# Kernel optimization log

Measured on AMD Instinct MI355X. Metric: run time of the kernel, lower is better.

The kernel has to match this reference:

```python
import jax, jax.numpy as jnp
import numpy as np

B, N, D = 4, 4096, 1024
H, DH = 16, 64  # heads, dim_head; inner_dim = H*DH = 1024
EPS = 1e-6


def setup_inputs() -> dict:
    key = jax.random.key(0)
    ks = jax.random.split(key, 6)
    s = 1.0 / np.sqrt(D)
    return {
        "x": jax.random.normal(ks[0], (B, N, D), dtype=jnp.float32),
        "Wq": jax.random.normal(ks[1], (D, H * DH), dtype=jnp.float32) * s,
        "Wk": jax.random.normal(ks[2], (D, H * DH), dtype=jnp.float32) * s,
        "Wv": jax.random.normal(ks[3], (D, H * DH), dtype=jnp.float32) * s,
        "Wo": jax.random.normal(ks[4], (H * DH, D), dtype=jnp.float32) * s,
        "bo": jnp.zeros((D,), dtype=jnp.float32),
    }


def reference(x, Wq, Wk, Wv, Wo, bo):
    # projections, split heads: b n (h d) -> b h n d
    def split_heads(t):
        b, n, _ = t.shape
        return t.reshape(b, n, H, DH).transpose(0, 2, 1, 3)

    q = split_heads(x @ Wq)
    k = split_heads(x @ Wk)  # context = x (self-attention)
    v = split_heads(x @ Wv)

    # elu feature map: elu(x) + 1
    q = jax.nn.elu(q) + 1.0
    k = jax.nn.elu(k) + 1.0

    # normalizer z[b,h,n,1] = q . sum_n k  + eps
    k_sum = k.sum(axis=2)                                  # b h d
    z = jnp.einsum('bhnd,bhd->bhn', q, k_sum)[..., None] + EPS

    # kv outer-product reduction: O(N d^2)
    kv = jnp.einsum('bhnd,bhne->bhde', k, v)               # b h d e
    out = jnp.einsum('bhnd,bhde->bhne', q, kv) / z         # b h n e

    # merge heads: b h n d -> b n (h d)
    out = out.transpose(0, 2, 1, 3).reshape(x.shape[0], x.shape[1], H * DH)
    return out @ Wo + bo
```

## Files before the change

kernel.cpp:

```cpp
#include <hip/hip_runtime.h>
#include <hip/hip_bf16.h>


#define DEV_INLINE __device__ __forceinline__

typedef short bf16x8 __attribute__((ext_vector_type(8)));
typedef float f32x4  __attribute__((ext_vector_type(4)));

static constexpr int Bb = 4, Nn = 4096, Dd = 1024, Hh = 16, DHd = 64;
static constexpr int Mrows = Bb * Nn;

DEV_INLINE float bf2f(short s) {
  unsigned u = ((unsigned)(unsigned short)s) << 16;
  float f; __builtin_memcpy(&f, &u, 4); return f;
}
DEV_INLINE short f2bf(float f) {
  unsigned u; __builtin_memcpy(&u, &f, 4);
  unsigned r = (u + 0x7fffu + ((u >> 16) & 1u)) >> 16;
  return (short)r;
}

DEV_INLINE void gload16(const void* g, void* l) {
  typedef __attribute__((address_space(1))) const void gv_t;
  typedef __attribute__((address_space(3))) void lv_t;
  __builtin_amdgcn_global_load_lds((gv_t*)g, (lv_t*)l, 16, 0, 0);
}

#define SBAR() __builtin_amdgcn_s_barrier()
#define WAITV(n) asm volatile("s_waitcnt vmcnt(" #n ")" ::: "memory")


__global__ void convert_x_kernel(const float* __restrict__ x, short* __restrict__ xb) {
  const int total = Mrows * 1024 / 4;
  for (int i = blockIdx.x * 256 + threadIdx.x; i < total; i += 2048 * 256) {
    float4 v = ((const float4*)x)[i];
    short4 o;
    o.x = f2bf(v.x); o.y = f2bf(v.y); o.z = f2bf(v.z); o.w = f2bf(v.w);
    ((short4*)xb)[i] = o;
  }
}

__global__ void transposeW_kernel(const float* __restrict__ Wq, const float* __restrict__ Wk,
                                  const float* __restrict__ Wv, const float* __restrict__ Wo,
                                  short* __restrict__ Wt, short* __restrict__ WoT) {
  int z = blockIdx.z;
  const float* W = (z == 0) ? Wq : (z == 1) ? Wk : (z == 2) ? Wv : Wo;
  short* dstb = (z < 3) ? (Wt + (size_t)z * 1024 * 1024) : WoT;
  __shared__ float tile[64][69];
  int t = threadIdx.x;
  int r = t >> 2, c4 = (t & 3) << 4;
  const float* src = W + (blockIdx.y * 64 + r) * 1024 + blockIdx.x * 64 + c4;
  for (int j = 0; j < 4; ++j) {
    float4 v = ((const float4*)src)[j];
    tile[r][c4 + 4 * j + 0] = v.x;
    tile[r][c4 + 4 * j + 1] = v.y;
    tile[r][c4 + 4 * j + 2] = v.z;
    tile[r][c4 + 4 * j + 3] = v.w;
  }
  __syncthreads();
  __attribute__((aligned(16))) short tmp[16];
  for (int j = 0; j < 16; ++j) tmp[j] = f2bf(tile[c4 + j][r]);
  short* dst = dstb + (blockIdx.x * 64 + r) * 1024 + blockIdx.y * 64 + c4;
  ((int4*)dst)[0] = ((int4*)tmp)[0];
  ((int4*)dst)[1] = ((int4*)tmp)[1];
}


DEV_INLINE void stage_half(const short* __restrict__ gtile, char* smreg, int h) {
  int t = threadIdx.x;
  int lane = t & 63, w = t >> 6;
#pragma unroll
  for (int l = 0; l < 2; ++l) {
    int rbase = h * 128 + l * 64 + w * 8;
    int row = rbase + (lane >> 3);
    int slot = lane & 7;
    gload16(gtile + (size_t)row * 1024 + ((slot ^ (row & 7)) << 3),
            smreg + (size_t)rbase * 128);
  }
}

#define READ_A(set, mbase, kk)                                                     \
  _Pragma("unroll") for (int m_ = 0; m_ < 4; ++m_) {                               \
    int row_ = wr * 128 + ((mbase) + m_) * 16 + rl;                                \
    int slot_ = (kk) * 4 + kg;                                                     \
    a[m_] = *(const bf16x8*)(smraw + (set) * 65536 + row_ * 128 +                  \
                             (((slot_ ^ (row_ & 7))) << 4));                       \
  }

#define READ_B(set, kk)                                                            \
  _Pragma("unroll") for (int n_ = 0; n_ < 4; ++n_) {                               \
    int row_ = wc * 64 + n_ * 16 + rl;                                             \
    int slot_ = (kk) * 4 + kg;                                                     \
    b[n_] = *(const bf16x8*)(smraw + 32768 + (set) * 65536 + row_ * 128 +          \
                             (((slot_ ^ (row_ & 7))) << 4));                       \
  }

#define MF(mbase)                                                                  \
  __builtin_amdgcn_s_setprio(1);                                                   \
  _Pragma("unroll") for (int m_ = 0; m_ < 4; ++m_)                                 \
    _Pragma("unroll") for (int n_ = 0; n_ < 4; ++n_)                               \
      acc[(mbase) + m_][n_] = __builtin_amdgcn_mfma_f32_16x16x32_bf16(             \
          a[m_], b[n_], acc[(mbase) + m_][n_], 0, 0, 0);                           \
  __builtin_amdgcn_s_setprio(0);

template <int MODE>
__global__ __launch_bounds__(512, 2) void gemm256_kernel(
    const short* __restrict__ A, const short* __restrict__ Bt,
    short* __restrict__ q, short* __restrict__ kT, short* __restrict__ vT,
    float* __restrict__ out, const float* __restrict__ bias, int nTilesN) {
  __shared__ __align__(16) char smraw[131072];
  char* smA0 = smraw;
  char* smB0 = smraw + 32768;
  char* smA1 = smraw + 65536;
  char* smB1 = smraw + 98304;

  int bid = blockIdx.x;
  int xcd = bid & 7, lo = bid >> 3;
  int tn = lo >> 3, tmg = lo & 7;
  int tm = xcd * 8 + tmg;

  int t = threadIdx.x, w = t >> 6, lane = t & 63;
  int rl = lane & 15, kg = lane >> 4;
  int wr = w >> 2, wc = w & 3;

  const short* Ab = A + (size_t)tm * 256 * 1024;
  const short* Bb2 = Bt + (size_t)tn * 256 * 1024;

  f32x4 acc[8][4] = {};
  bf16x8 a[4], b[4];

  stage_half(Ab, smA0, 0);
  stage_half(Ab, smA0, 1);
  stage_half(Bb2, smB0, 0);
  stage_half(Bb2, smB0, 1);
  stage_half(Bb2 + 64, smB1, 0);
  WAITV(2);
  SBAR();

#pragma unroll 1
  for (int i = 0; i < 8; ++i) {
    int k_odd = i * 128 + 64, k_n2 = i * 128 + 128, k_n3 = i * 128 + 192;
    READ_A(0, 0, 0); READ_B(0, 0);
    stage_half(Bb2 + k_odd, smB1, 1);
    SBAR(); MF(0); SBAR();
    READ_A(0, 4, 0);
    stage_half(Ab + k_odd, smA1, 0);
    SBAR(); MF(4); SBAR();
    READ_A(0, 0, 1); READ_B(0, 1);
    stage_half(Ab + k_odd, smA1, 1);
    SBAR(); MF(0); SBAR();
    READ_A(0, 4, 1);
    stage_half(Bb2 + k_n2, smB0, 0);
    WAITV(2); SBAR(); MF(4); SBAR();
    READ_A(1, 0, 0); READ_B(1, 0);
    stage_half(Ab + k_n2, smA0, 0);
    SBAR(); MF(0); SBAR();
    READ_A(1, 4, 0);
    stage_half(Ab + k_n2, smA0, 1);
    SBAR(); MF(4); SBAR();
    READ_A(1, 0, 1); READ_B(1, 1);
    stage_half(Bb2 + k_n2, smB0, 1);
    SBAR(); MF(0); SBAR();
    READ_A(1, 4, 1);
    stage_half(Bb2 + k_n3, smB1, 0);
    WAITV(2); SBAR(); MF(4); SBAR();
  }

  WAITV(0);
  SBAR();

  if (MODE == 1) {
    float* smf = (float*)smraw;
    for (int hp = 0; hp < 2; ++hp) {
      if (wr == hp) {
#pragma unroll
        for (int m = 0; m < 8; ++m)
#pragma unroll
          for (int n = 0; n < 4; ++n)
#pragma unroll
            for (int r = 0; r < 4; ++r) {
              int lrow = m * 16 + kg * 4 + r;
              int col = wc * 64 + n * 16 + rl;
              smf[lrow * 256 + ((((col >> 2) ^ (lrow & 7))) << 2) + (col & 3)] = acc[m][n][r];
            }
      }
      SBAR();
      for (int it = 0; it < 16; ++it) {
        int idx = it * 512 + t;
        int row = idx >> 6, c4 = (idx & 63) << 2;
        float4 v = *(const float4*)&smf[row * 256 + ((((c4 >> 2) ^ (row & 7))) << 2)];
        float4 bv = *(const float4*)&bias[tn * 256 + c4];
        v.x += bv.x; v.y += bv.y; v.z += bv.z; v.w += bv.w;
        *(float4*)&out[(size_t)(tm * 256 + hp * 128 + row) * Dd + tn * 256 + c4] = v;
      }
      SBAR();
    }
    return;
  }

  short* smc = (short*)smraw;
  int sec = tn >> 2, tl = tn & 3;
#pragma unroll
  for (int m = 0; m < 8; ++m)
#pragma unroll
    for (int n = 0; n < 4; ++n)
#pragma unroll
      for (int r = 0; r < 4; ++r) {
        float v = acc[m][n][r];
        if (sec <= 1) v = v > 0.f ? v + 1.f : __expf(v);
        int row = wr * 128 + m * 16 + kg * 4 + r;
        int col = wc * 64 + n * 16 + rl;
        int rr = (sec == 0) ? row : col;
        int cc = (sec == 0) ? col : row;
        smc[rr * 256 + ((((cc >> 3) ^ (rr & 7))) << 3) + (cc & 7)] = f2bf(v);
      }
  SBAR();
  if (sec == 0) {
    for (int it = 0; it < 16; ++it) {
      int idx = it * 512 + t;
      int row = idx >> 5, c8 = (idx & 31) << 3;
      int4 val = *(const int4*)&smc[row * 256 + ((((c8 >> 3) ^ (row & 7))) << 3)];
      int grow = tm * 256 + row;
      int bI = grow >> 12, n = grow & 4095;
      int g = tl * 256 + c8;
      int h = g >> 6, d0 = g & 63;
      *(int4*)&q[(((size_t)(bI * Hh + h)) * Nn + n) * DHd + d0] = val;
    }
  } else {
    short* dst = (sec == 1) ? kT : vT;
    for (int it = 0; it < 16; ++it) {
      int idx = it * 512 + t;
      int dr = idx >> 5, c8 = (idx & 31) << 3;
      int4 val = *(const int4*)&smc[dr * 256 + ((((c8 >> 3) ^ (dr & 7))) << 3)];
      int g = tl * 256 + dr;
      int h = g >> 6, d = g & 63;
      int grow0 = tm * 256 + c8;
      int bI = grow0 >> 12, n0 = grow0 & 4095;
      *(int4*)&dst[(((size_t)(bI * Hh + h)) * DHd + d) * Nn + n0] = val;
    }
  }
}

__global__ void ksum_kernel(const short* __restrict__ kT, float* __restrict__ ksp) {
  int bh = blockIdx.x >> 3, seg = blockIdx.x & 7;
  int t = threadIdx.x;
  int d = t >> 2, sub = t & 3;
  const short* row = kT + ((size_t)bh * DHd + d) * Nn + seg * 512;
  float s = 0.f;
  for (int i = sub * 8; i < 512; i += 32) {
    bf16x8 v = *(const bf16x8*)&row[i];
    for (int j = 0; j < 8; ++j) s += bf2f(v[j]);
  }
  s += __shfl_xor(s, 1);
  s += __shfl_xor(s, 2);
  if (sub == 0) ksp[(bh * 8 + seg) * 64 + d] = s;
}

__global__ __launch_bounds__(256, 2) void kv_kernel(const short* __restrict__ kT,
                                                    const short* __restrict__ vT,
                                                    float* __restrict__ kvp) {
  __shared__ __align__(16) short smK[64 * 128];
  __shared__ __align__(16) short smV[64 * 128];
  int bh = blockIdx.x, seg = blockIdx.y;
  int t = threadIdx.x;
  int w = t >> 6, lane = t & 63, rl = lane & 15, kg = lane >> 4;
  const short* kb = kT + (size_t)bh * DHd * Nn + seg * 1024;
  const short* vb = vT + (size_t)bh * DHd * Nn + seg * 1024;
  f32x4 acc[4] = {};
  for (int n0 = 0; n0 < 1024; n0 += 128) {
    __syncthreads();
    for (int p = 0; p < 4; ++p) {
      int c = p * 256 + t;
      int row = c >> 4, u = c & 15;
      int off = ((u ^ (row & 15)) << 3);
      gload16(kb + row * Nn + n0 + off, (char*)smK + p * 4096 + w * 1024);
      gload16(vb + row * Nn + n0 + off, (char*)smV + p * 4096 + w * 1024);
    }
    __syncthreads();
    for (int kk = 0; kk < 4; ++kk) {
      int slot = kk * 4 + kg;
      int rowA = w * 16 + rl;
      bf16x8 a = *(const bf16x8*)&smK[rowA * 128 + ((slot ^ (rowA & 15)) << 3)];
      for (int nt = 0; nt < 4; ++nt) {
        int rowB = nt * 16 + rl;
        bf16x8 b = *(const bf16x8*)&smV[rowB * 128 + ((slot ^ (rowB & 15)) << 3)];
        acc[nt] = __builtin_amdgcn_mfma_f32_16x16x32_bf16(a, b, acc[nt], 0, 0, 0);
      }
    }
  }
  float* smf = (float*)smK;
  __syncthreads();
  for (int nt = 0; nt < 4; ++nt)
    for (int r = 0; r < 4; ++r)
      smf[(nt * 16 + rl) * 64 + (w * 16 + kg * 4 + r)] = acc[nt][r];
  __syncthreads();
  float* dst = kvp + ((size_t)(bh * 4 + seg)) * 4096;
  for (int i = 0; i < 4; ++i) {
    int idx = i * 256 + t;
    int e = idx >> 4, c4 = (idx & 15) << 2;
    *(float4*)&dst[e * 64 + c4] = *(const float4*)&smf[e * 64 + c4];
  }
}

__global__ void kvc_kernel(const float* __restrict__ kvp, short* __restrict__ kvT) {
  int bh = blockIdx.x, t = threadIdx.x;
  const float* p0 = kvp + (size_t)bh * 4 * 4096;
  for (int rep = 0; rep < 4; ++rep) {
    int idx = rep * 1024 + t * 4;
    float4 a = *(const float4*)&p0[idx];
    float4 b = *(const float4*)&p0[4096 + idx];
    float4 c = *(const float4*)&p0[8192 + idx];
    float4 d = *(const float4*)&p0[12288 + idx];
    short4 o;
    o.x = f2bf(a.x + b.x + c.x + d.x);
    o.y = f2bf(a.y + b.y + c.y + d.y);
    o.z = f2bf(a.z + b.z + c.z + d.z);
    o.w = f2bf(a.w + b.w + c.w + d.w);
    *(short4*)&kvT[(size_t)bh * 4096 + idx] = o;
  }
}

__global__ __launch_bounds__(256, 2) void attn_kernel(const short* __restrict__ q,
                                                      const short* __restrict__ kvT,
                                                      const float* __restrict__ ksp,
                                                      short* __restrict__ attn) {
  int rb = blockIdx.x, bh = blockIdx.y;
  int b = bh >> 4, h = bh & 15;
  __shared__ float sks[64];
  __shared__ __align__(16) short satt[64 * 64];
  int t = threadIdx.x, w = t >> 6, lane = t & 63, rl = lane & 15, kg = lane >> 4;
  if (t < 64) {
    float s = 0.f;
    for (int j = 0; j < 8; ++j) s += ksp[(bh * 8 + j) * 64 + t];
    sks[t] = s;
  }
  __syncthreads();
  int row0 = rb * 64 + w * 16;
  const short* qb = q + ((size_t)bh * Nn + row0) * DHd;
  const short* kvb = kvT + (size_t)bh * 4096;
  f32x4 acc[4] = {};
  float zp = 0.f;
  for (int kk = 0; kk < 2; ++kk) {
    int kb = kk * 32 + kg * 8;
    bf16x8 a = *(const bf16x8*)&qb[rl * DHd + kb];
    for (int j = 0; j < 8; ++j) zp += bf2f(a[j]) * sks[kb + j];
    for (int nt = 0; nt < 4; ++nt) {
      bf16x8 bfr = *(const bf16x8*)&kvb[(nt * 16 + rl) * 64 + kb];
      acc[nt] = __builtin_amdgcn_mfma_f32_16x16x32_bf16(a, bfr, acc[nt], 0, 0, 0);
    }
  }
  zp += __shfl_xor(zp, 16);
  zp += __shfl_xor(zp, 32);
  float zr[4];
  for (int r = 0; r < 4; ++r) zr[r] = __shfl(zp, kg * 4 + r);
  for (int nt = 0; nt < 4; ++nt)
    for (int r = 0; r < 4; ++r)
      satt[(w * 16 + kg * 4 + r) * 64 + nt * 16 + rl] = f2bf(acc[nt][r] / (zr[r] + 1e-6f));
  __syncthreads();
  for (int i = 0; i < 2; ++i) {
    int idx = i * 256 + t;
    int row = idx >> 3, c8 = (idx & 7) << 3;
    int n = rb * 64 + row;
    *(int4*)&attn[((size_t)(b * Nn + n)) * 1024 + h * 64 + c8] = *(const int4*)&satt[row * 64 + c8];
  }
}

extern "C" void kernel_launch(void* const* d_in, const int* in_sizes, int n_in,
                              void* d_out, int out_size, void* d_ws, size_t ws_size,
                              hipStream_t stream) {
  const float* x  = (const float*)d_in[0];
  const float* Wq = (const float*)d_in[1];
  const float* Wk = (const float*)d_in[2];
  const float* Wv = (const float*)d_in[3];
  const float* Wo = (const float*)d_in[4];
  const float* bo = (const float*)d_in[5];
  float* out = (float*)d_out;

  char* ws = (char*)d_ws;
  size_t off = 0;
  auto alloc = [&](size_t bytes) {
    char* p = ws + off;
    off += (bytes + 255) & ~(size_t)255;
    return p;
  };
  short* xb   = (short*)alloc((size_t)Mrows * 1024 * 2);
  short* Wt   = (short*)alloc((size_t)3072 * 1024 * 2);
  short* WoT  = (short*)alloc((size_t)1024 * 1024 * 2);
  short* qb   = (short*)alloc((size_t)64 * Nn * DHd * 2);
  short* kT   = (short*)alloc((size_t)64 * DHd * Nn * 2);
  short* vT   = (short*)alloc((size_t)64 * DHd * Nn * 2);
  float* ksp  = (float*)alloc((size_t)64 * 8 * 64 * 4);
  float* kvp  = (float*)alloc((size_t)64 * 4 * 4096 * 4);
  short* kvT  = (short*)alloc((size_t)64 * 4096 * 2);
  short* attn = (short*)alloc((size_t)Mrows * 1024 * 2);
  (void)alloc(8192);

  convert_x_kernel<<<2048, 256, 0, stream>>>(x, xb);
  transposeW_kernel<<<dim3(16, 16, 4), 256, 0, stream>>>(Wq, Wk, Wv, Wo, Wt, WoT);

  gemm256_kernel<0><<<768, 512, 0, stream>>>(xb, Wt, qb, kT, vT, nullptr, nullptr, 12);
  ksum_kernel<<<512, 256, 0, stream>>>(kT, ksp);
  kv_kernel<<<dim3(64, 4), 256, 0, stream>>>(kT, vT, kvp);
  kvc_kernel<<<64, 256, 0, stream>>>(kvp, kvT);
  attn_kernel<<<dim3(64, 64), 256, 0, stream>>>(qb, kvT, ksp, attn);
  gemm256_kernel<1><<<256, 512, 0, stream>>>(attn, WoT, nullptr, nullptr, nullptr, out, bo, 4);
}
```

Baseline: 250.7 us.

## Fuse k-sum into QKV GEMM epilogue, precompute LDS addresses, split kv over more blocks

The k column sum moves into the QKV GEMM epilogue, which accumulates it with atomics into a buffer zeroed by the weight-transpose kernel. This removes the separate ksum kernel and its re-read of kT. The GEMM main loop now uses precomputed swizzled LDS base pointers and global offsets, cutting address arithmetic per tile step. The kv reduction is split into 8 segments instead of 4 for more parallelism, at the cost of a larger partial buffer to combine. Float atomics make the k sum order nondeterministic.

Measured after the change: 250.1 us. No clear change (-0.3%).

```diff
diff --git a/kernel.cpp b/kernel.cpp
--- a/kernel.cpp
+++ b/kernel.cpp
@@ -42,12 +42,15 @@
 
 __global__ void transposeW_kernel(const float* __restrict__ Wq, const float* __restrict__ Wk,
                                   const float* __restrict__ Wv, const float* __restrict__ Wo,
-                                  short* __restrict__ Wt, short* __restrict__ WoT) {
+                                  short* __restrict__ Wt, short* __restrict__ WoT,
+                                  float* __restrict__ ksum) {
   int z = blockIdx.z;
+  int t = threadIdx.x;
+  if (z == 0 && blockIdx.y == 0 && blockIdx.x < 16)
+    ksum[blockIdx.x * 256 + t] = 0.f;
   const float* W = (z == 0) ? Wq : (z == 1) ? Wk : (z == 2) ? Wv : Wo;
   short* dstb = (z < 3) ? (Wt + (size_t)z * 1024 * 1024) : WoT;
   __shared__ float tile[64][69];
-  int t = threadIdx.x;
   int r = t >> 2, c4 = (t & 3) << 4;
   const float* src = W + (blockIdx.y * 64 + r) * 1024 + blockIdx.x * 64 + c4;
   for (int j = 0; j < 4; ++j) {
@@ -66,53 +69,33 @@
 }
 
 
-DEV_INLINE void stage_half(const short* __restrict__ gtile, char* smreg, int h) {
-  int t = threadIdx.x;
-  int lane = t & 63, w = t >> 6;
-#pragma unroll
-  for (int l = 0; l < 2; ++l) {
-    int rbase = h * 128 + l * 64 + w * 8;
-    int row = rbase + (lane >> 3);
-    int slot = lane & 7;
-    gload16(gtile + (size_t)row * 1024 + ((slot ^ (row & 7)) << 3),
-            smreg + (size_t)rbase * 128);
-  }
-}
-
-#define READ_A(set, mbase, kk)                                                     \
-  _Pragma("unroll") for (int m_ = 0; m_ < 4; ++m_) {                               \
-    int row_ = wr * 128 + ((mbase) + m_) * 16 + rl;                                \
-    int slot_ = (kk) * 4 + kg;                                                     \
-    a[m_] = *(const bf16x8*)(smraw + (set) * 65536 + row_ * 128 +                  \
-                             (((slot_ ^ (row_ & 7))) << 4));                       \
-  }
-
-#define READ_B(set, kk)                                                            \
-  _Pragma("unroll") for (int n_ = 0; n_ < 4; ++n_) {                               \
-    int row_ = wc * 64 + n_ * 16 + rl;                                             \
-    int slot_ = (kk) * 4 + kg;                                                     \
-    b[n_] = *(const bf16x8*)(smraw + 32768 + (set) * 65536 + row_ * 128 +          \
-                             (((slot_ ^ (row_ & 7))) << 4));                       \
-  }
-
-#define MF(mbase)                                                                  \
-  __builtin_amdgcn_s_setprio(1);                                                   \
-  _Pragma("unroll") for (int m_ = 0; m_ < 4; ++m_)                                 \
-    _Pragma("unroll") for (int n_ = 0; n_ < 4; ++n_)                               \
-      acc[(mbase) + m_][n_] = __builtin_amdgcn_mfma_f32_16x16x32_bf16(             \
-          a[m_], b[n_], acc[(mbase) + m_][n_], 0, 0, 0);                           \
+#define RA(set, mbase, kk)                                                   \
+  _Pragma("unroll") for (int m_ = 0; m_ < 4; ++m_)                           \
+    a[m_] = *(const bf16x8*)(baseA##set##kk + ((mbase) + m_) * 2048);
+
+#define RB(set, kk)                                                          \
+  _Pragma("unroll") for (int n_ = 0; n_ < 4; ++n_)                           \
+    b[n_] = *(const bf16x8*)(baseB##set##kk + n_ * 2048);
+
+#define MF(mbase)                                                            \
+  __builtin_amdgcn_s_setprio(1);                                             \
+  _Pragma("unroll") for (int m_ = 0; m_ < 4; ++m_)                           \
+    _Pragma("unroll") for (int n_ = 0; n_ < 4; ++n_)                         \
+      acc[(mbase) + m_][n_] = __builtin_amdgcn_mfma_f32_16x16x32_bf16(       \
+          a[m_], b[n_], acc[(mbase) + m_][n_], 0, 0, 0);                     \
   __builtin_amdgcn_s_setprio(0);
+
+#define STG(Gb, t, h, reg)                                                   \
+  gload16((Gb) + (t) * 64 + (h) * 131072 + goff,         (reg) + (h) * 16384 + wq);          \
+  gload16((Gb) + (t) * 64 + (h) * 131072 + 65536 + goff, (reg) + (h) * 16384 + 8192 + wq);
 
 template <int MODE>
 __global__ __launch_bounds__(512, 2) void gemm256_kernel(
     const short* __restrict__ A, const short* __restrict__ Bt,
     short* __restrict__ q, short* __restrict__ kT, short* __restrict__ vT,
-    float* __restrict__ out, const float* __restrict__ bias, int nTilesN) {
+    float* __restrict__ out, const float* __restrict__ bias,
+    float* __restrict__ ksum, int nTilesN) {
   __shared__ __align__(16) char smraw[131072];
-  char* smA0 = smraw;
-  char* smB0 = smraw + 32768;
-  char* smA1 = smraw + 65536;
-  char* smB1 = smraw + 98304;
 
   int bid = blockIdx.x;
   int xcd = bid & 7, lo = bid >> 3;
@@ -126,43 +109,59 @@
   const short* Ab = A + (size_t)tm * 256 * 1024;
   const short* Bb2 = Bt + (size_t)tn * 256 * 1024;
 
+  const int rx = rl & 7;
+  char* baseA00 = smraw + (wr * 128 + rl) * 128 + (((0 * 4 + kg) ^ rx) << 4);
+  char* baseA01 = smraw + (wr * 128 + rl) * 128 + (((1 * 4 + kg) ^ rx) << 4);
+  char* baseA10 = baseA00 + 65536;
+  char* baseA11 = baseA01 + 65536;
+  char* baseB00 = smraw + 32768 + (wc * 64 + rl) * 128 + (((0 * 4 + kg) ^ rx) << 4);
+  char* baseB01 = smraw + 32768 + (wc * 64 + rl) * 128 + (((1 * 4 + kg) ^ rx) << 4);
+  char* baseB10 = baseB00 + 65536;
+  char* baseB11 = baseB01 + 65536;
+
+  int srow = w * 8 + (lane >> 3);
+  const int goff = srow * 1024 + (((lane & 7) ^ (srow & 7)) << 3);
+  const int wq = w * 1024;
+  char* regA0 = smraw;
+  char* regB0 = smraw + 32768;
+  char* regA1 = smraw + 65536;
+  char* regB1 = smraw + 98304;
+
   f32x4 acc[8][4] = {};
   bf16x8 a[4], b[4];
 
-  stage_half(Ab, smA0, 0);
-  stage_half(Ab, smA0, 1);
-  stage_half(Bb2, smB0, 0);
-  stage_half(Bb2, smB0, 1);
-  stage_half(Bb2 + 64, smB1, 0);
+  STG(Ab, 0, 0, regA0); STG(Ab, 0, 1, regA0);
+  STG(Bb2, 0, 0, regB0); STG(Bb2, 0, 1, regB0);
+  STG(Bb2, 1, 0, regB1);
   WAITV(2);
   SBAR();
 
 #pragma unroll 1
   for (int i = 0; i < 8; ++i) {
-    int k_odd = i * 128 + 64, k_n2 = i * 128 + 128, k_n3 = i * 128 + 192;
-    READ_A(0, 0, 0); READ_B(0, 0);
-    stage_half(Bb2 + k_odd, smB1, 1);
+    int t1 = 2 * i + 1, t2 = 2 * i + 2, t3 = 2 * i + 3;
+    RA(0, 0, 0); RB(0, 0);
+    STG(Bb2, t1, 1, regB1);
     SBAR(); MF(0); SBAR();
-    READ_A(0, 4, 0);
-    stage_half(Ab + k_odd, smA1, 0);
+    RA(0, 4, 0);
+    STG(Ab, t1, 0, regA1);
     SBAR(); MF(4); SBAR();
-    READ_A(0, 0, 1); READ_B(0, 1);
-    stage_half(Ab + k_odd, smA1, 1);
+    RA(0, 0, 1); RB(0, 1);
+    STG(Ab, t1, 1, regA1);
     SBAR(); MF(0); SBAR();
-    READ_A(0, 4, 1);
-    stage_half(Bb2 + k_n2, smB0, 0);
+    RA(0, 4, 1);
+    STG(Bb2, t2, 0, regB0);
     WAITV(2); SBAR(); MF(4); SBAR();
-    READ_A(1, 0, 0); READ_B(1, 0);
-    stage_half(Ab + k_n2, smA0, 0);
+    RA(1, 0, 0); RB(1, 0);
+    STG(Ab, t2, 0, regA0);
     SBAR(); MF(0); SBAR();
-    READ_A(1, 4, 0);
-    stage_half(Ab + k_n2, smA0, 1);
+    RA(1, 4, 0);
+    STG(Ab, t2, 1, regA0);
     SBAR(); MF(4); SBAR();
-    READ_A(1, 0, 1); READ_B(1, 1);
-    stage_half(Bb2 + k_n2, smB0, 1);
+    RA(1, 0, 1); RB(1, 1);
+    STG(Bb2, t2, 1, regB0);
     SBAR(); MF(0); SBAR();
-    READ_A(1, 4, 1);
-    stage_half(Bb2 + k_n3, smB1, 0);
+    RA(1, 4, 1);
+    STG(Bb2, t3, 0, regB1);
     WAITV(2); SBAR(); MF(4); SBAR();
   }
 
@@ -238,22 +237,20 @@
       int bI = grow0 >> 12, n0 = grow0 & 4095;
       *(int4*)&dst[(((size_t)(bI * Hh + h)) * DHd + d) * Nn + n0] = val;
     }
-  }
-}
-
-__global__ void ksum_kernel(const short* __restrict__ kT, float* __restrict__ ksp) {
-  int bh = blockIdx.x >> 3, seg = blockIdx.x & 7;
-  int t = threadIdx.x;
-  int d = t >> 2, sub = t & 3;
-  const short* row = kT + ((size_t)bh * DHd + d) * Nn + seg * 512;
-  float s = 0.f;
-  for (int i = sub * 8; i < 512; i += 32) {
-    bf16x8 v = *(const bf16x8*)&row[i];
-    for (int j = 0; j < 8; ++j) s += bf2f(v[j]);
-  }
-  s += __shfl_xor(s, 1);
-  s += __shfl_xor(s, 2);
-  if (sub == 0) ksp[(bh * 8 + seg) * 64 + d] = s;
+    if (sec == 1) {
+      int dcol = t >> 1, half = t & 1;
+      float s = 0.f;
+      for (int c = half * 128; c < half * 128 + 128; ++c)
+        s += bf2f(smc[dcol * 256 + ((((c >> 3) ^ (dcol & 7))) << 3) + (c & 7)]);
+      s += __shfl_xor(s, 1);
+      if (half == 0) {
+        int g = tl * 256 + dcol;
+        int h = g >> 6, d = g & 63;
+        int bI = (tm * 256) >> 12;
+        atomicAdd(&ksum[(bI * Hh + h) * DHd + d], s);
+      }
+    }
+  }
 }
 
 __global__ __launch_bounds__(256, 2) void kv_kernel(const short* __restrict__ kT,
@@ -264,10 +261,10 @@
   int bh = blockIdx.x, seg = blockIdx.y;
   int t = threadIdx.x;
   int w = t >> 6, lane = t & 63, rl = lane & 15, kg = lane >> 4;
-  const short* kb = kT + (size_t)bh * DHd * Nn + seg * 1024;
-  const short* vb = vT + (size_t)bh * DHd * Nn + seg * 1024;
+  const short* kb = kT + (size_t)bh * DHd * Nn + seg * 512;
+  const short* vb = vT + (size_t)bh * DHd * Nn + seg * 512;
   f32x4 acc[4] = {};
-  for (int n0 = 0; n0 < 1024; n0 += 128) {
+  for (int n0 = 0; n0 < 512; n0 += 128) {
     __syncthreads();
     for (int p = 0; p < 4; ++p) {
       int c = p * 256 + t;
@@ -280,11 +277,11 @@
     for (int kk = 0; kk < 4; ++kk) {
       int slot = kk * 4 + kg;
       int rowA = w * 16 + rl;
-      bf16x8 a = *(const bf16x8*)&smK[rowA * 128 + ((slot ^ (rowA & 15)) << 3)];
+      bf16x8 av = *(const bf16x8*)&smK[rowA * 128 + ((slot ^ (rowA & 15)) << 3)];
       for (int nt = 0; nt < 4; ++nt) {
         int rowB = nt * 16 + rl;
-        bf16x8 b = *(const bf16x8*)&smV[rowB * 128 + ((slot ^ (rowB & 15)) << 3)];
-        acc[nt] = __builtin_amdgcn_mfma_f32_16x16x32_bf16(a, b, acc[nt], 0, 0, 0);
+        bf16x8 bv = *(const bf16x8*)&smV[rowB * 128 + ((slot ^ (rowB & 15)) << 3)];
+        acc[nt] = __builtin_amdgcn_mfma_f32_16x16x32_bf16(av, bv, acc[nt], 0, 0, 0);
       }
     }
   }
@@ -294,7 +291,7 @@
     for (int r = 0; r < 4; ++r)
       smf[(nt * 16 + rl) * 64 + (w * 16 + kg * 4 + r)] = acc[nt][r];
   __syncthreads();
-  float* dst = kvp + ((size_t)(bh * 4 + seg)) * 4096;
+  float* dst = kvp + ((size_t)(bh * 8 + seg)) * 4096;
   for (int i = 0; i < 4; ++i) {
     int idx = i * 256 + t;
     int e = idx >> 4, c4 = (idx & 15) << 2;
@@ -304,36 +301,30 @@
 
 __global__ void kvc_kernel(const float* __restrict__ kvp, short* __restrict__ kvT) {
   int bh = blockIdx.x, t = threadIdx.x;
-  const float* p0 = kvp + (size_t)bh * 4 * 4096;
+  const float* p0 = kvp + (size_t)bh * 8 * 4096;
   for (int rep = 0; rep < 4; ++rep) {
     int idx = rep * 1024 + t * 4;
-    float4 a = *(const float4*)&p0[idx];
-    float4 b = *(const float4*)&p0[4096 + idx];
-    float4 c = *(const float4*)&p0[8192 + idx];
-    float4 d = *(const float4*)&p0[12288 + idx];
+    float4 s = *(const float4*)&p0[idx];
+    for (int j = 1; j < 8; ++j) {
+      float4 aa = *(const float4*)&p0[j * 4096 + idx];
+      s.x += aa.x; s.y += aa.y; s.z += aa.z; s.w += aa.w;
+    }
     short4 o;
-    o.x = f2bf(a.x + b.x + c.x + d.x);
-    o.y = f2bf(a.y + b.y + c.y + d.y);
-    o.z = f2bf(a.z + b.z + c.z + d.z);
-    o.w = f2bf(a.w + b.w + c.w + d.w);
+    o.x = f2bf(s.x); o.y = f2bf(s.y); o.z = f2bf(s.z); o.w = f2bf(s.w);
     *(short4*)&kvT[(size_t)bh * 4096 + idx] = o;
   }
 }
 
 __global__ __launch_bounds__(256, 2) void attn_kernel(const short* __restrict__ q,
                                                       const short* __restrict__ kvT,
-                                                      const float* __restrict__ ksp,
+                                                      const float* __restrict__ ksum,
                                                       short* __restrict__ attn) {
   int rb = blockIdx.x, bh = blockIdx.y;
   int b = bh >> 4, h = bh & 15;
   __shared__ float sks[64];
   __shared__ __align__(16) short satt[64 * 64];
   int t = threadIdx.x, w = t >> 6, lane = t & 63, rl = lane & 15, kg = lane >> 4;
-  if (t < 64) {
-    float s = 0.f;
-    for (int j = 0; j < 8; ++j) s += ksp[(bh * 8 + j) * 64 + t];
-    sks[t] = s;
-  }
+  if (t < 64) sks[t] = ksum[bh * 64 + t];
   __syncthreads();
   int row0 = rb * 64 + w * 16;
   const short* qb = q + ((size_t)bh * Nn + row0) * DHd;
@@ -342,11 +333,11 @@
   float zp = 0.f;
   for (int kk = 0; kk < 2; ++kk) {
     int kb = kk * 32 + kg * 8;
-    bf16x8 a = *(const bf16x8*)&qb[rl * DHd + kb];
-    for (int j = 0; j < 8; ++j) zp += bf2f(a[j]) * sks[kb + j];
+    bf16x8 av = *(const bf16x8*)&qb[rl * DHd + kb];
+    for (int j = 0; j < 8; ++j) zp += bf2f(av[j]) * sks[kb + j];
     for (int nt = 0; nt < 4; ++nt) {
       bf16x8 bfr = *(const bf16x8*)&kvb[(nt * 16 + rl) * 64 + kb];
-      acc[nt] = __builtin_amdgcn_mfma_f32_16x16x32_bf16(a, bfr, acc[nt], 0, 0, 0);
+      acc[nt] = __builtin_amdgcn_mfma_f32_16x16x32_bf16(av, bfr, acc[nt], 0, 0, 0);
     }
   }
   zp += __shfl_xor(zp, 16);
@@ -389,19 +380,18 @@
   short* qb   = (short*)alloc((size_t)64 * Nn * DHd * 2);
   short* kT   = (short*)alloc((size_t)64 * DHd * Nn * 2);
   short* vT   = (short*)alloc((size_t)64 * DHd * Nn * 2);
-  float* ksp  = (float*)alloc((size_t)64 * 8 * 64 * 4);
-  float* kvp  = (float*)alloc((size_t)64 * 4 * 4096 * 4);
+  float* ksum = (float*)alloc((size_t)64 * 64 * 4);
+  float* kvp  = (float*)alloc((size_t)64 * 8 * 4096 * 4);
   short* kvT  = (short*)alloc((size_t)64 * 4096 * 2);
   short* attn = (short*)alloc((size_t)Mrows * 1024 * 2);
-  (void)alloc(8192);
+  (void)alloc(1 << 20);
 
   convert_x_kernel<<<2048, 256, 0, stream>>>(x, xb);
-  transposeW_kernel<<<dim3(16, 16, 4), 256, 0, stream>>>(Wq, Wk, Wv, Wo, Wt, WoT);
-
-  gemm256_kernel<0><<<768, 512, 0, stream>>>(xb, Wt, qb, kT, vT, nullptr, nullptr, 12);
-  ksum_kernel<<<512, 256, 0, stream>>>(kT, ksp);
-  kv_kernel<<<dim3(64, 4), 256, 0, stream>>>(kT, vT, kvp);
+  transposeW_kernel<<<dim3(16, 16, 4), 256, 0, stream>>>(Wq, Wk, Wv, Wo, Wt, WoT, ksum);
+
+  gemm256_kernel<0><<<768, 512, 0, stream>>>(xb, Wt, qb, kT, vT, nullptr, nullptr, ksum, 12);
+  kv_kernel<<<dim3(64, 8), 256, 0, stream>>>(kT, vT, kvp);
   kvc_kernel<<<64, 256, 0, stream>>>(kvp, kvT);
-  attn_kernel<<<dim3(64, 64), 256, 0, stream>>>(qb, kvT, ksp, attn);
-  gemm256_kernel<1><<<256, 512, 0, stream>>>(attn, WoT, nullptr, nullptr, nullptr, out, bo, 4);
-}
+  attn_kernel<<<dim3(64, 64), 256, 0, stream>>>(qb, kvT, ksum, attn);
+  gemm256_kernel<1><<<256, 512, 0, stream>>>(attn, WoT, nullptr, nullptr, nullptr, out, bo, nullptr, 4);
+}
```
